# Kernel optimization log

Hardware: AMD Instinct MI355X
Metric: run time of the kernel (lower is better)

Reference implementation:

```python
import jax, jax.numpy as jnp
import numpy as np

D_MODEL = 256
SEQ_L = 4096
BATCH = 8
H = 3 * D_MODEL   # inner width after 3-branch concat
N_STATE = 32      # complex conjugate pairs -> d_state=64 real
KSIZES = (3, 7, 15)
DILATIONS = (1, 2, 4)


def setup_inputs() -> dict:
    k = jax.random.split(jax.random.key(0), 16)
    d = D_MODEL
    def w(ki, shape, scale):
        return jax.random.normal(ki, shape, jnp.float32) * scale
    inp = {"x": jax.random.normal(k[0], (BATCH, SEQ_L, d), jnp.float32)}
    for i, ksz in enumerate(KSIZES):
        inp[f"conv_w{i}"] = w(k[1 + i], (d, d, ksz), (d * ksz) ** -0.5)
        inp[f"conv_b{i}"] = jnp.zeros((d,), jnp.float32)
    inp["gate_w"] = w(k[4], (H, d), d ** -0.5)
    inp["gate_b"] = jnp.zeros((H,), jnp.float32)
    inp["res_w"] = w(k[5], (H, d), d ** -0.5)
    inp["res_b"] = jnp.zeros((H,), jnp.float32)
    # S4D (diagonal SSM) parameters, d_state=64 -> 32 complex pairs
    inp["log_dt"] = jax.random.uniform(k[6], (H,), jnp.float32, np.log(0.001), np.log(0.1))
    inp["A_re"] = -0.5 * jnp.ones((H, N_STATE), jnp.float32)
    inp["A_im"] = jnp.broadcast_to(np.pi * jnp.arange(N_STATE, dtype=jnp.float32), (H, N_STATE)).copy()
    inp["C_re"] = w(k[7], (H, N_STATE), 0.2)
    inp["C_im"] = w(k[8], (H, N_STATE), 0.2)
    inp["Dskip"] = jax.random.normal(k[9], (H,), jnp.float32)
    inp["ln_gamma"] = jnp.ones((H,), jnp.float32)
    inp["ln_beta"] = jnp.zeros((H,), jnp.float32)
    return inp


def _dil_conv(u, w, b, dil):
    # u: [B, C, L], w: [O, I, K], torch 'same' padding (odd kernels)
    y = jax.lax.conv_general_dilated(
        u, w, window_strides=(1,), padding="SAME", rhs_dilation=(dil,),
        dimension_numbers=("NCH", "OIH", "NCH"))
    return y + b[None, :, None]


def _s4d_apply(u, log_dt, A_re, A_im, C_re, C_im, Dskip):
    # u: [B, H, L]; diagonal SSM long convolution via FFT (ZOH discretization)
    L = u.shape[-1]
    dt = jnp.exp(log_dt)                          # [H]
    A = A_re + 1j * A_im                          # [H, N]
    C = C_re + 1j * C_im                          # [H, N]
    dtA = dt[:, None] * A                         # [H, N]
    C_disc = C * (jnp.exp(dtA) - 1.0) / A         # ZOH input matrix folded into C
    t = jnp.arange(L, dtype=jnp.float32)
    vand = jnp.exp(dtA[:, :, None] * t)           # [H, N, L] Vandermonde
    kern = 2.0 * jnp.real(jnp.einsum("hn,hnl->hl", C_disc, vand))  # [H, L]
    n_fft = 2 * L
    kf = jnp.fft.rfft(kern, n_fft)                # [H, n_fft/2+1]
    uf = jnp.fft.rfft(u, n_fft)                   # [B, H, n_fft/2+1]
    y = jnp.fft.irfft(uf * kf[None], n_fft)[..., :L]
    return y + Dskip[None, :, None] * u


def reference(x, conv_w0, conv_b0, conv_w1, conv_b1, conv_w2, conv_b2,
              gate_w, gate_b, res_w, res_b,
              log_dt, A_re, A_im, C_re, C_im, Dskip, ln_gamma, ln_beta):
    u = jnp.transpose(x, (0, 2, 1))               # [B, d, L]
    convs = [
        _dil_conv(u, conv_w0, conv_b0, DILATIONS[0]),
        _dil_conv(u, conv_w1, conv_b1, DILATIONS[1]),
        _dil_conv(u, conv_w2, conv_b2, DILATIONS[2]),
    ]
    combined = jnp.concatenate(convs, axis=1)     # [B, 3d, L]
    gate = jax.nn.sigmoid(jnp.einsum("bdl,od->bol", u, gate_w) + gate_b[None, :, None])
    gated = combined * gate
    s4_out = _s4d_apply(gated, log_dt, A_re, A_im, C_re, C_im, Dskip)
    resid = jnp.einsum("bdl,od->bol", u, res_w) + res_b[None, :, None]
    out = jnp.transpose(s4_out + resid, (0, 2, 1))  # [B, L, 3d]
    mu = jnp.mean(out, axis=-1, keepdims=True)
    var = jnp.mean((out - mu) ** 2, axis=-1, keepdims=True)
    return (out - mu) * jax.lax.rsqrt(var + 1e-5) * ln_gamma + ln_beta
```

## Files before the change

### kernel.cpp

```cpp
#include <hip/hip_runtime.h>
#include <cstdint>
#include <cstddef>


#define B_ 8
#define L_ 4096
#define D_ 256
#define H_ 768
#define NST 32
#define LC 128
#define NC 32

typedef _Float16 f16;
typedef _Float16 f16x8 __attribute__((ext_vector_type(8)));
typedef _Float16 f16x4 __attribute__((ext_vector_type(4)));
typedef _Float16 f16x2 __attribute__((ext_vector_type(2)));
typedef float f32x4 __attribute__((ext_vector_type(4)));

__device__ __forceinline__ f32x4 mfma16(f16x8 a, f16x8 b, f32x4 c) {
  return __builtin_amdgcn_mfma_f32_16x16x32_f16(a, b, c, 0, 0, 0);
}

#define GLDS16(g, l)                                                              \
  __builtin_amdgcn_global_load_lds((const __attribute__((address_space(1))) void*)(g), \
                                   (__attribute__((address_space(3))) void*)(l), 16, 0, 0)

__global__ __launch_bounds__(256) void prep_all(
    const float* __restrict__ x, const float* __restrict__ gate_w,
    const float* __restrict__ res_w,
    const float* __restrict__ w0, const float* __restrict__ w1, const float* __restrict__ w2,
    f16* __restrict__ xh, f16* __restrict__ Ag, float* __restrict__ zbuf,
    f16* __restrict__ A) {
  int bid = blockIdx.x, tid = threadIdx.x;
  if (bid < 8192) {
    int i = (bid * 256 + tid) * 4;
    float4 v = *(const float4*)(x + i);
    xh[i+0]=(f16)v.x; xh[i+1]=(f16)v.y; xh[i+2]=(f16)v.z; xh[i+3]=(f16)v.w;
  } else if (bid < 8384) {
    int i = ((bid - 8192) * 256 + tid) * 4;
    float4 v = *(const float4*)(gate_w + i);
    Ag[i+0]=(f16)v.x; Ag[i+1]=(f16)v.y; Ag[i+2]=(f16)v.z; Ag[i+3]=(f16)v.w;
  } else if (bid < 8576) {
    int i = ((bid - 8384) * 256 + tid) * 4;
    float4 v = *(const float4*)(res_w + i);
    f16* d = Ag + 768 * 256;
    d[i+0]=(f16)v.x; d[i+1]=(f16)v.y; d[i+2]=(f16)v.z; d[i+3]=(f16)v.w;
  } else if (bid == 8576) {
    zbuf[tid] = 0.f;
  } else {
    int idx = (bid - 8577) * 256 + tid;
    const int n0 = 256 * 256 * 3, n1 = 256 * 256 * 7;
    const float* w; int K, base;
    if (idx < n0) { w = w0; K = 3; base = 0; }
    else if (idx < n0 + n1) { idx -= n0; w = w1; K = 7; base = 256 * 768; }
    else { idx -= n0 + n1; w = w2; K = 15; base = 256 * 768 + 256 * 1792; }
    int o = idx / (256 * K); int r = idx - o * (256 * K); int j = r / K; int t = r - j * K;
    A[base + o * (256 * K) + t * 256 + j] = (f16)w[idx];
  }
}

__global__ __launch_bounds__(256) void s4_all(const float* __restrict__ log_dt,
                                              const float* __restrict__ A_re,
                                              const float* __restrict__ A_im,
                                              const float* __restrict__ C_re,
                                              const float* __restrict__ C_im,
                                              f16* __restrict__ A1, f16* __restrict__ A2,
                                              float* __restrict__ WLc,
                                              float* __restrict__ kT) {
  int bid = blockIdx.x, tid = threadIdx.x;
  if (bid < 96) {
    int idx = bid * 256 + tid;
    int h = idx >> 5, n = idx & 31;
    float dt = expf(log_dt[h]);
    float Ar = A_re[idx], Ai = A_im[idx];
    float ar = dt * Ar, ai = dt * Ai;
    float e = expf(ar), sn, cs; sincosf(ai, &sn, &cs);
    float wr = e * cs, wi = e * sn;
    float den = Ar * Ar + Ai * Ai;
    float Er = wr - 1.f, Ei = wi;
    float Cr = C_re[idx], Ci = C_im[idx];
    float nr = Cr * Er - Ci * Ei, ni = Cr * Ei + Ci * Er;
    float Cdr = (nr * Ar + ni * Ai) / den;
    float Cdi = (ni * Ar - nr * Ai) / den;
    f16* A1r = A1 + ((size_t)h * 64 + 2 * n) * LC;
    f16* A1i = A1 + ((size_t)h * 64 + 2 * n + 1) * LC;
    float pr = 1.f, pi = 0.f;
    for (int j = 0; j < LC; ++j) {
      A1r[LC - 1 - j] = (f16)pr; A1i[LC - 1 - j] = (f16)pi;
      float t0 = pr * wr - pi * wi; pi = pr * wi + pi * wr; pr = t0;
    }
    WLc[idx * 2] = pr; WLc[idx * 2 + 1] = pi;
    float qr = wr, qi = wi;
    for (int t = 0; t < LC; ++t) {
      A2[((size_t)h * LC + t) * 64 + 2 * n]     = (f16)(2.f * (Cdr * qr - Cdi * qi));
      A2[((size_t)h * LC + t) * 64 + 2 * n + 1] = (f16)(-2.f * (Cdr * qi + Cdi * qr));
      float t0 = qr * wr - qi * wi; qi = qr * wi + qi * wr; qr = t0;
    }
  } else {
    int idx = (bid - 96) * 256 + tid;
    int h = idx >> 7, j = idx & 127;
    float dt = expf(log_dt[h]);
    float acc = 0.f;
    for (int n = 0; n < NST; ++n) {
      float Ar = A_re[h * 32 + n], Ai = A_im[h * 32 + n];
      float ar = dt * Ar, ai = dt * Ai;
      float e1 = expf(ar), s1, c1; sincosf(ai, &s1, &c1);
      float wr = e1 * c1, wi = e1 * s1;
      float den = Ar * Ar + Ai * Ai;
      float Er = wr - 1.f, Ei = wi;
      float Cr = C_re[h * 32 + n], Ci = C_im[h * 32 + n];
      float nr = Cr * Er - Ci * Ei, ni = Cr * Ei + Ci * Er;
      float Cdr = (nr * Ar + ni * Ai) / den, Cdi = (ni * Ar - nr * Ai) / den;
      float ej = expf(ar * (float)j), sj, cj; sincosf(ai * (float)j, &sj, &cj);
      acc += 2.f * (Cdr * (ej * cj) - Cdi * (ej * sj));
    }
    kT[idx] = acc;
  }
}

__global__ __launch_bounds__(256) void gemm_gr(
    const f16* __restrict__ xh, const f16* __restrict__ Agr,
    const float* __restrict__ gate_b, const float* __restrict__ res_b,
    f16* __restrict__ gts, f16* __restrict__ res) {
  __shared__ f16 As[128 * 64];
  __shared__ f16 Bs[128 * 64];
  const int mt = blockIdx.y, nt = blockIdx.x;
  const int b = nt >> 5, l0 = (nt & 31) * 128;
  const bool isg = mt < 6;
  const int hbase = (isg ? mt : mt - 6) * 128;
  const f16* Abase = Agr + (size_t)((isg ? 0 : 768) + hbase) * 256;
  const int tid = threadIdx.x;
  const int wid = tid >> 6, lane = tid & 63, l15 = lane & 15, quad = lane >> 4;
  const int wm = (wid & 1) * 64, wn = (wid >> 1) * 64;
  const int srow = (wid << 5) + (lane >> 3);
  const int sperm = ((lane & 7) ^ (lane >> 3)) << 3;
  char* AsL = (char*)As + (wid << 12);
  char* BsL = (char*)Bs + (wid << 12);
  const f16* xrow = xh + (((size_t)b * L_) << 8);

  f32x4 acc[4][4];
#pragma unroll
  for (int i = 0; i < 4; ++i)
#pragma unroll
    for (int j = 0; j < 4; ++j) acc[i][j] = (f32x4){0.f, 0.f, 0.f, 0.f};

  for (int kc = 0; kc < 4; ++kc) {
#pragma unroll
    for (int j = 0; j < 4; ++j) {
      int row = srow + j * 8;
      GLDS16(Abase + (size_t)row * 256 + kc * 64 + sperm, AsL + (j << 10));
      GLDS16(xrow + ((size_t)(l0 + row) << 8) + kc * 64 + sperm, BsL + (j << 10));
    }
    __syncthreads();
#pragma unroll
    for (int k2 = 0; k2 < 2; ++k2) {
      f16x8 af[4], bf[4];
#pragma unroll
      for (int mi = 0; mi < 4; ++mi) {
        int r = wm + mi * 16 + l15;
        af[mi] = *(const f16x8*)(&As[r * 64 + (((k2 * 4 + quad) ^ (r & 7)) << 3)]);
      }
#pragma unroll
      for (int ni = 0; ni < 4; ++ni) {
        int r = wn + ni * 16 + l15;
        bf[ni] = *(const f16x8*)(&Bs[r * 64 + (((k2 * 4 + quad) ^ (r & 7)) << 3)]);
      }
#pragma unroll
      for (int mi = 0; mi < 4; ++mi)
#pragma unroll
        for (int ni = 0; ni < 4; ++ni) acc[mi][ni] = mfma16(af[mi], bf[ni], acc[mi][ni]);
    }
    __syncthreads();
  }

  if (isg) {
#pragma unroll
    for (int mi = 0; mi < 4; ++mi)
#pragma unroll
      for (int ni = 0; ni < 4; ++ni) {
        int hg = hbase + wm + mi * 16 + quad * 4;
        int lg = l0 + wn + ni * 16 + l15;
#pragma unroll
        for (int r = 0; r < 4; ++r) {
          float val = acc[mi][ni][r] + gate_b[hg + r];
          gts[((size_t)(b * H_ + hg + r)) * L_ + lg] = (f16)(1.f / (1.f + expf(-val)));
        }
      }
  } else {
#pragma unroll
    for (int mi = 0; mi < 4; ++mi)
#pragma unroll
      for (int ni = 0; ni < 4; ++ni) {
        int hg = hbase + wm + mi * 16 + quad * 4;
        int lg = l0 + wn + ni * 16 + l15;
#pragma unroll
        for (int r = 0; r < 4; ++r)
          res[((size_t)(b * H_ + hg + r)) * L_ + lg] = (f16)(acc[mi][ni][r] + res_b[hg + r]);
      }
  }
}

__global__ __launch_bounds__(512, 2) void gemm_conv8(
    const f16* __restrict__ xh, const f16* __restrict__ Aconv,
    const float* __restrict__ cb0, const float* __restrict__ cb1, const float* __restrict__ cb2,
    const f16* __restrict__ gts, const f16* __restrict__ zbuf,
    f16* __restrict__ v) {
  __shared__ f16 lds[69632];
  f16* Bs = lds + 49152;

  const int nt = blockIdx.x;
  const int b = nt >> 4, l0 = (nt & 15) * 256;
  const int ci = 2 - blockIdx.y;
  const int tid = threadIdx.x;
  const int wid = tid >> 6, lane = tid & 63, l15 = lane & 15, quad = lane >> 4;
  const int wr = wid >> 2, wc = wid & 3;
  const int rq = tid >> 3;
  const int cswz = ((tid & 7) ^ ((tid >> 3) & 7)) << 3;
  const f16* xrow = xh + (((size_t)b * L_) << 8);

  const f16* Acb; int Krow, taps, dil;
  if (ci == 0)      { Acb = Aconv;                          Krow = 768;  taps = 3;  dil = 1; }
  else if (ci == 1) { Acb = Aconv + 256 * 768;              Krow = 1792; taps = 7;  dil = 2; }
  else              { Acb = Aconv + 256 * 768 + 256 * 1792; Krow = 3840; taps = 15; dil = 4; }
  const int S = taps * 4;
  const int half = (taps - 1) / 2;

  f32x4 acc[8][4];
#pragma unroll
  for (int i = 0; i < 8; ++i)
#pragma unroll
    for (int j = 0; j < 4; ++j) acc[i][j] = (f32x4){0.f, 0.f, 0.f, 0.f};
  f16x8 af[4][2], blo[2][2], bhi[2][2];

  auto stageB = [&](int jc) {
#pragma unroll
    for (int q = 0; q < 5; ++q) {
      int r = q * 64 + rq;
      int gl = l0 - 32 + r;
      const f16* src = (gl < 0 || gl >= L_) ? (zbuf + cswz)
                       : xrow + ((size_t)gl << 8) + jc * 64 + cswz;
      GLDS16(src, Bs + q * 4096 + wid * 512);
    }
  };
  auto stageA2 = [&](int t2, int jc2, f16* buf, int q0) {
#pragma unroll
    for (int q = q0; q < q0 + 2; ++q) {
      const f16* src = Acb + (size_t)(q * 64 + rq) * Krow + t2 * 256 + jc2 * 64 + cswz;
      GLDS16(src, buf + q * 4096 + wid * 512);
    }
  };
  auto loadA = [&](const f16* Ab, int MH) {
#pragma unroll
    for (int mi = 0; mi < 4; ++mi) {
      int r = MH * 128 + wr * 64 + mi * 16 + l15;
#pragma unroll
      for (int k2 = 0; k2 < 2; ++k2)
        af[mi][k2] = *(const f16x8*)(Ab + r * 64 + (((k2 * 4 + quad) ^ (r & 7)) << 3));
    }
  };
  auto loadB = [&](int NH, int shift, f16x8 (&bf)[2][2]) {
#pragma unroll
    for (int ni = 0; ni < 2; ++ni) {
      int r = shift + NH * 128 + wc * 32 + ni * 16 + l15;
#pragma unroll
      for (int k2 = 0; k2 < 2; ++k2)
        bf[ni][k2] = *(const f16x8*)(Bs + r * 64 + (((k2 * 4 + quad) ^ (r & 7)) << 3));
    }
  };
  auto quadMM = [&](int MH, int NH, f16x8 (&bf)[2][2]) {
#pragma unroll
    for (int k2 = 0; k2 < 2; ++k2)
#pragma unroll
      for (int mi = 0; mi < 4; ++mi)
#pragma unroll
        for (int ni = 0; ni < 2; ++ni)
          acc[MH * 4 + mi][NH * 2 + ni] =
              mfma16(af[mi][k2], bf[ni][k2], acc[MH * 4 + mi][NH * 2 + ni]);
  };

  stageB(0);
  stageA2(0, 0, lds, 0);           stageA2(0, 0, lds, 2);
  stageA2(1, 0, lds + 16384, 0);   stageA2(1, 0, lds + 16384, 2);
  asm volatile("s_waitcnt vmcnt(0)" ::: "memory");
  __builtin_amdgcn_s_barrier();

  int s = 0, ca = 0;
#pragma unroll 1
  for (int jc = 0; jc < 4; ++jc) {
    if (jc > 0) {
      stageB(jc);
      asm volatile("s_waitcnt vmcnt(0)" ::: "memory");
      __builtin_amdgcn_s_barrier();
    }
#pragma unroll 1
    for (int t = 0; t < taps; ++t, ++s) {
      const int shift = 32 + (t - half) * dil;
      f16* Acur = lds + ca * 16384;
      int pa = ca - 1; if (pa < 0) pa = 2;
      f16* Apre = lds + pa * 16384;
      int t2 = t + 2, jc2 = jc;
      if (t2 >= taps) { t2 -= taps; ++jc2; }
      const bool pf = (jc2 < 4);
      loadA(Acur, 0); loadB(0, shift, blo);
      if (pf) stageA2(t2, jc2, Apre, 0);
      __builtin_amdgcn_s_barrier();
      asm volatile("s_waitcnt lgkmcnt(0)" ::: "memory");
      __builtin_amdgcn_s_setprio(1);
      quadMM(0, 0, blo);
      __builtin_amdgcn_s_setprio(0);
      __builtin_amdgcn_s_barrier();
      loadB(1, shift, bhi);
      if (pf) stageA2(t2, jc2, Apre, 2);
      __builtin_amdgcn_s_barrier();
      asm volatile("s_waitcnt lgkmcnt(0)" ::: "memory");
      __builtin_amdgcn_s_setprio(1);
      quadMM(0, 1, bhi);
      __builtin_amdgcn_s_setprio(0);
      __builtin_amdgcn_s_barrier();
      loadA(Acur, 1);
      __builtin_amdgcn_s_barrier();
      asm volatile("s_waitcnt lgkmcnt(0)" ::: "memory");
      __builtin_amdgcn_s_setprio(1);
      quadMM(1, 1, bhi);
      __builtin_amdgcn_s_setprio(0);
      __builtin_amdgcn_s_barrier();
      __builtin_amdgcn_s_setprio(1);
      quadMM(1, 0, blo);
      __builtin_amdgcn_s_setprio(0);
      if (pf) asm volatile("s_waitcnt vmcnt(4)" ::: "memory");
      else    asm volatile("s_waitcnt vmcnt(0)" ::: "memory");
      __builtin_amdgcn_s_barrier();
      ca = (ca == 2) ? 0 : ca + 1;
    }
  }

  const float* cbias = (ci == 0) ? cb0 : (ci == 1 ? cb1 : cb2);
#pragma unroll
  for (int mh = 0; mh < 2; ++mh)
#pragma unroll
    for (int mi = 0; mi < 4; ++mi)
#pragma unroll
      for (int nh = 0; nh < 2; ++nh)
#pragma unroll
        for (int ni = 0; ni < 2; ++ni) {
          int mg = mh * 128 + wr * 64 + mi * 16 + quad * 4;
          int lg = l0 + nh * 128 + wc * 32 + ni * 16 + l15;
          f32x4 a4 = acc[mh * 4 + mi][nh * 2 + ni];
#pragma unroll
          for (int r = 0; r < 4; ++r) {
            size_t a = ((size_t)(b * H_ + ci * 256 + mg + r)) * L_ + lg;
            float val = (a4[r] + cbias[mg + r]) * (float)gts[a];
            v[a] = (f16)val;
          }
        }
}

__global__ __launch_bounds__(256) void s1_states(const f16* __restrict__ v,
                                                 const f16* __restrict__ A1,
                                                 const float* __restrict__ WLc,
                                                 f16* __restrict__ Xin) {
  __shared__ f16 A1s[64 * 136];
  __shared__ f16 Vs[128 * 136];
  const int h = blockIdx.y, cb = blockIdx.x;
  const int tid = threadIdx.x;
  {
    int row = tid >> 2, q = tid & 3;
    const f16x8* src = (const f16x8*)(A1 + ((size_t)h * 64 + row) * 128 + q * 32);
    f16x8* dst = (f16x8*)(&A1s[row * 136 + q * 32]);
    dst[0] = src[0]; dst[1] = src[1]; dst[2] = src[2]; dst[3] = src[3];
  }
  {
    int col = tid >> 1, half = tid & 1;
    int cg = cb * 128 + col, b = cg >> 5, c = cg & 31;
    const f16x8* src = (const f16x8*)(v + ((size_t)(b * H_ + h)) * L_ + c * 128 + half * 64);
    f16x8* dst = (f16x8*)(&Vs[col * 136 + half * 64]);
    dst[0] = src[0]; dst[1] = src[1]; dst[2] = src[2]; dst[3] = src[3];
    dst[4] = src[4]; dst[5] = src[5]; dst[6] = src[6]; dst[7] = src[7];
  }
  __syncthreads();
  const int wid = tid >> 6, lane = tid & 63, l15 = lane & 15, quad = lane >> 4;
  const int n0 = wid * 32;
  f32x4 acc[4][2];
#pragma unroll
  for (int i = 0; i < 4; ++i) { acc[i][0] = (f32x4){0,0,0,0}; acc[i][1] = (f32x4){0,0,0,0}; }
#pragma unroll
  for (int bk = 0; bk < 4; ++bk) {
    f16x8 af[4], bf[2];
#pragma unroll
    for (int mi = 0; mi < 4; ++mi)
      af[mi] = *(const f16x8*)(&A1s[(mi * 16 + l15) * 136 + bk * 32 + quad * 8]);
#pragma unroll
    for (int ni = 0; ni < 2; ++ni)
      bf[ni] = *(const f16x8*)(&Vs[(n0 + ni * 16 + l15) * 136 + bk * 32 + quad * 8]);
#pragma unroll
    for (int mi = 0; mi < 4; ++mi)
#pragma unroll
      for (int ni = 0; ni < 2; ++ni) acc[mi][ni] = mfma16(af[mi], bf[ni], acc[mi][ni]);
  }
  __syncthreads();
  float* Xls = (float*)Vs;
#pragma unroll
  for (int mi = 0; mi < 4; ++mi)
#pragma unroll
    for (int ni = 0; ni < 2; ++ni) {
      int col = n0 + ni * 16 + l15;
      *(f32x4*)(&Xls[col * 68 + mi * 16 + quad * 4]) = acc[mi][ni];
    }
  __syncthreads();
  if (tid < 128) {
    int b4 = tid >> 5, n = tid & 31;
    int b = cb * 4 + b4;
    float Wr = WLc[(h * NST + n) * 2], Wi = WLc[(h * NST + n) * 2 + 1];
    float xr = 0.f, xi = 0.f;
    f16* xout = Xin + (((size_t)(b * H_ + h)) * NC) * 64 + 2 * n;
    for (int c = 0; c < NC; ++c) {
      float er = Xls[(b4 * 32 + c) * 68 + 2 * n];
      float ei = Xls[(b4 * 32 + c) * 68 + 2 * n + 1];
      f16x2 o; o[0] = (f16)xr; o[1] = (f16)xi;
      *(f16x2*)(xout + (size_t)c * 64) = o;
      float t = Wr * xr - Wi * xi + er;
      xi = Wr * xi + Wi * xr + ei; xr = t;
    }
  }
}

__global__ __launch_bounds__(256) void s3_output(const f16* __restrict__ v,
                                                 const f16* __restrict__ A2g,
                                                 const f16* __restrict__ res,
                                                 const float* __restrict__ kT,
                                                 const f16* __restrict__ Xin,
                                                 const float* __restrict__ Dskip,
                                                 f16* __restrict__ y4) {
  __shared__ f16 Ts[128 * 136];
  __shared__ f16 Vs[64 * 136];
  __shared__ float kTs[128];
  f16* A2s = Ts;
  f16* Xs = Ts + 128 * 72;
  const int h = blockIdx.y, cb = blockIdx.x;
  const int tid = threadIdx.x;
  if (tid < 128) kTs[tid] = kT[h * 128 + tid];
  {
    int col = tid >> 2, q = tid & 3;
    int cg = cb * 64 + col, b = cg >> 5, c = cg & 31;
    const f16x8* src = (const f16x8*)(v + ((size_t)(b * H_ + h)) * L_ + c * 128 + q * 32);
    f16x8* dst = (f16x8*)(&Vs[col * 136 + q * 32]);
    dst[0] = src[0]; dst[1] = src[1]; dst[2] = src[2]; dst[3] = src[3];
  }
  __syncthreads();
  {
    int tau = tid >> 1, h64 = (tid & 1) * 64;
#pragma unroll
    for (int jv = 0; jv < 8; ++jv) {
      int s0 = h64 + jv * 8;
      f16x8 w;
#pragma unroll
      for (int e = 0; e < 8; ++e) {
        int s = s0 + e;
        w[e] = (f16)((s <= tau) ? kTs[tau - s] : 0.f);
      }
      *(f16x8*)(&Ts[tau * 136 + s0]) = w;
    }
  }
  __syncthreads();
  const int wid = tid >> 6, lane = tid & 63, l15 = lane & 15, quad = lane >> 4;
  const int wm = (wid & 1) * 64, wn = (wid >> 1) * 32;
  f32x4 acc[4][2];
#pragma unroll
  for (int i = 0; i < 4; ++i) { acc[i][0] = (f32x4){0,0,0,0}; acc[i][1] = (f32x4){0,0,0,0}; }
#pragma unroll
  for (int bk = 0; bk < 4; ++bk) {
    f16x8 af[4], bf[2];
#pragma unroll
    for (int mi = 0; mi < 4; ++mi)
      af[mi] = *(const f16x8*)(&Ts[(wm + mi * 16 + l15) * 136 + bk * 32 + quad * 8]);
#pragma unroll
    for (int ni = 0; ni < 2; ++ni)
      bf[ni] = *(const f16x8*)(&Vs[(wn + ni * 16 + l15) * 136 + bk * 32 + quad * 8]);
#pragma unroll
    for (int mi = 0; mi < 4; ++mi)
#pragma unroll
      for (int ni = 0; ni < 2; ++ni) acc[mi][ni] = mfma16(af[mi], bf[ni], acc[mi][ni]);
  }
  __syncthreads();
  {
    int row = tid >> 1, half = tid & 1;
    const f16x8* src = (const f16x8*)(A2g + ((size_t)h * 128 + row) * 64 + half * 32);
    f16x8* dst = (f16x8*)(&A2s[row * 72 + half * 32]);
    dst[0] = src[0]; dst[1] = src[1]; dst[2] = src[2]; dst[3] = src[3];
  }
  {
    int col = tid >> 2, part = tid & 3;
    int cg = cb * 64 + col, b = cg >> 5, c = cg & 31;
    const f16x8* src = (const f16x8*)(Xin + (((size_t)(b * H_ + h)) * NC + c) * 64 + part * 16);
    f16x8* dst = (f16x8*)(&Xs[col * 72 + part * 16]);
    dst[0] = src[0]; dst[1] = src[1];
  }
  __syncthreads();
#pragma unroll
  for (int bk = 0; bk < 2; ++bk) {
    f16x8 af[4], bf[2];
#pragma unroll
    for (int mi = 0; mi < 4; ++mi)
      af[mi] = *(const f16x8*)(&A2s[(wm + mi * 16 + l15) * 72 + bk * 32 + quad * 8]);
#pragma unroll
    for (int ni = 0; ni < 2; ++ni)
      bf[ni] = *(const f16x8*)(&Xs[(wn + ni * 16 + l15) * 72 + bk * 32 + quad * 8]);
#pragma unroll
    for (int mi = 0; mi < 4; ++mi)
#pragma unroll
      for (int ni = 0; ni < 2; ++ni) acc[mi][ni] = mfma16(af[mi], bf[ni], acc[mi][ni]);
  }
  float Dh = Dskip[h];
#pragma unroll
  for (int mi = 0; mi < 4; ++mi)
#pragma unroll
    for (int ni = 0; ni < 2; ++ni) {
      int col = wn + ni * 16 + l15;
      int cg = cb * 64 + col, b = cg >> 5, c = cg & 31;
      int tau0 = wm + mi * 16 + quad * 4;
      size_t lbase = ((size_t)(b * H_ + h)) * L_ + c * 128 + tau0;
      const f16* rp = res + lbase;
      f16x4 o;
#pragma unroll
      for (int r = 0; r < 4; ++r)
        o[r] = (f16)(acc[mi][ni][r] + Dh * (float)Vs[col * 136 + tau0 + r] + (float)rp[r]);
      *(f16x4*)(y4 + lbase) = o;
    }
}

__global__ __launch_bounds__(256) void layernorm_t(const f16* __restrict__ y4,
                                                   const float* __restrict__ gamma,
                                                   const float* __restrict__ beta,
                                                   float* __restrict__ out) {
  __shared__ f16 Ys[768 * 72];
  __shared__ float psum[256], psq[256], mu[64], rs[64];
  const int b = blockIdx.y, l0 = blockIdx.x * 64;
  const int tid = threadIdx.x;
  {
    int r8 = tid >> 3, c = tid & 7;
    for (int it = 0; it < 24; ++it) {
      int hh = it * 32 + r8;
      f16x8 x = *(const f16x8*)(y4 + ((size_t)(b * H_ + hh)) * L_ + l0 + c * 8);
      *(f16x8*)(&Ys[hh * 72 + c * 8]) = x;
    }
  }
  __syncthreads();
  {
    int l = tid & 63, hg = tid >> 6;
    float s = 0.f, s2 = 0.f;
    for (int k = 0; k < 192; ++k) {
      float val = (float)Ys[(hg * 192 + k) * 72 + l];
      s += val; s2 += val * val;
    }
    psum[hg * 64 + l] = s; psq[hg * 64 + l] = s2;
  }
  __syncthreads();
  if (tid < 64) {
    float S = 0.f, S2 = 0.f;
    for (int g = 0; g < 4; ++g) { S += psum[g * 64 + tid]; S2 += psq[g * 64 + tid]; }
    float m = S / 768.f;
    float var = S2 / 768.f - m * m;
    mu[tid] = m; rs[tid] = rsqrtf(var + 1e-5f);
  }
  __syncthreads();
  float g0 = gamma[tid], g1 = gamma[256 + tid], g2 = gamma[512 + tid];
  float be0 = beta[tid], be1 = beta[256 + tid], be2 = beta[512 + tid];
  for (int lv = 0; lv < 8; ++lv) {
    f16x8 y0 = *(const f16x8*)(&Ys[(size_t)tid * 72 + lv * 8]);
    f16x8 y1 = *(const f16x8*)(&Ys[(size_t)(256 + tid) * 72 + lv * 8]);
    f16x8 y2 = *(const f16x8*)(&Ys[(size_t)(512 + tid) * 72 + lv * 8]);
#pragma unroll
    for (int e = 0; e < 8; ++e) {
      int ll = lv * 8 + e;
      float m = mu[ll], r = rs[ll];
      size_t ob = ((size_t)b * L_ + l0 + ll) * H_;
      out[ob + tid]       = ((float)y0[e] - m) * r * g0 + be0;
      out[ob + 256 + tid] = ((float)y1[e] - m) * r * g1 + be1;
      out[ob + 512 + tid] = ((float)y2[e] - m) * r * g2 + be2;
    }
  }
}

extern "C" void kernel_launch(void* const* d_in, const int* in_sizes, int n_in,
                              void* d_out, int out_size, void* d_ws, size_t ws_size,
                              hipStream_t stream) {
  const float* x      = (const float*)d_in[0];
  const float* cw0    = (const float*)d_in[1];
  const float* cb0    = (const float*)d_in[2];
  const float* cw1    = (const float*)d_in[3];
  const float* cb1    = (const float*)d_in[4];
  const float* cw2    = (const float*)d_in[5];
  const float* cb2    = (const float*)d_in[6];
  const float* gate_w = (const float*)d_in[7];
  const float* gate_b = (const float*)d_in[8];
  const float* res_w  = (const float*)d_in[9];
  const float* res_b  = (const float*)d_in[10];
  const float* log_dt = (const float*)d_in[11];
  const float* A_re   = (const float*)d_in[12];
  const float* A_im   = (const float*)d_in[13];
  const float* C_re   = (const float*)d_in[14];
  const float* C_im   = (const float*)d_in[15];
  const float* Dskip  = (const float*)d_in[16];
  const float* ln_g   = (const float*)d_in[17];
  const float* ln_b   = (const float*)d_in[18];
  float* out = (float*)d_out;

  char* ws = (char*)d_ws;
  f16*   xh   = (f16*)(ws + 0);
  f16*   Ac   = (f16*)(ws + 16777216);
  f16*   Ag   = (f16*)(ws + 20054016);
  f16*   zbuf = (f16*)(ws + 20840448);
  f16*   vb   = (f16*)(ws + 20841472);
  f16*   resb = (f16*)(ws + 71173120);
  f16*   gts  = (f16*)(ws + 121504768);
  f16*   A1   = (f16*)(ws + 171836416);
  f16*   A2   = (f16*)(ws + 184419328);
  float* kT   = (float*)(ws + 197002240);
  float* WLc  = (float*)(ws + 197395456);
  f16*   Xin  = (f16*)(ws + 197592064);
  f16*   y4   = (f16*)(ws + 222757888);

  prep_all<<<14977, 256, 0, stream>>>(x, gate_w, res_w, cw0, cw1, cw2,
                                      xh, Ag, (float*)zbuf, Ac);
  s4_all<<<480, 256, 0, stream>>>(log_dt, A_re, A_im, C_re, C_im, A1, A2, WLc, kT);

  gemm_gr<<<dim3(256, 12), 256, 0, stream>>>(xh, Ag, gate_b, res_b, gts, resb);
  gemm_conv8<<<dim3(128, 3), 512, 0, stream>>>(xh, Ac, cb0, cb1, cb2, gts, zbuf, vb);

  s1_states<<<dim3(2, 768), 256, 0, stream>>>(vb, A1, WLc, Xin);
  s3_output<<<dim3(4, 768), 256, 0, stream>>>(vb, A2, resb, kT, Xin, Dskip, y4);

  layernorm_t<<<dim3(64, 8), 256, 0, stream>>>(y4, ln_g, ln_b, out);
}
```

Before: 453.6 us.

## Remap conv GEMM warps to 4x2 tiling and software-pipeline B fragment reads

```diff
diff --git a/kernel.cpp b/kernel.cpp
--- a/kernel.cpp
+++ b/kernel.cpp
@@ -213,7 +213,7 @@
   const int ci = 2 - blockIdx.y;
   const int tid = threadIdx.x;
   const int wid = tid >> 6, lane = tid & 63, l15 = lane & 15, quad = lane >> 4;
-  const int wr = wid >> 2, wc = wid & 3;
+  const int wr = wid >> 1, wc = wid & 1;
   const int rq = tid >> 3;
   const int cswz = ((tid & 7) ^ ((tid >> 3) & 7)) << 3;
   const f16* xrow = xh + (((size_t)b * L_) << 8);
@@ -222,15 +222,15 @@
   if (ci == 0)      { Acb = Aconv;                          Krow = 768;  taps = 3;  dil = 1; }
   else if (ci == 1) { Acb = Aconv + 256 * 768;              Krow = 1792; taps = 7;  dil = 2; }
   else              { Acb = Aconv + 256 * 768 + 256 * 1792; Krow = 3840; taps = 15; dil = 4; }
-  const int S = taps * 4;
   const int half = (taps - 1) / 2;
-
-  f32x4 acc[8][4];
-#pragma unroll
-  for (int i = 0; i < 8; ++i)
-#pragma unroll
-    for (int j = 0; j < 4; ++j) acc[i][j] = (f32x4){0.f, 0.f, 0.f, 0.f};
-  f16x8 af[4][2], blo[2][2], bhi[2][2];
+  const int shift0 = 32 - half * dil;
+
+  f32x4 acc[4][8];
+#pragma unroll
+  for (int i = 0; i < 4; ++i)
+#pragma unroll
+    for (int j = 0; j < 8; ++j) acc[i][j] = (f32x4){0.f, 0.f, 0.f, 0.f};
+  f16x8 af[4][2], bfA[2][2], bfB[2][2];
 
   auto stageB = [&](int jc) {
 #pragma unroll
@@ -242,117 +242,104 @@
       GLDS16(src, Bs + q * 4096 + wid * 512);
     }
   };
-  auto stageA2 = [&](int t2, int jc2, f16* buf, int q0) {
-#pragma unroll
-    for (int q = q0; q < q0 + 2; ++q) {
+  auto stageA4 = [&](int t2, int jc2, f16* buf) {
+#pragma unroll
+    for (int q = 0; q < 4; ++q) {
       const f16* src = Acb + (size_t)(q * 64 + rq) * Krow + t2 * 256 + jc2 * 64 + cswz;
       GLDS16(src, buf + q * 4096 + wid * 512);
     }
   };
-  auto loadA = [&](const f16* Ab, int MH) {
+  auto readAF = [&](const f16* Ab) {
 #pragma unroll
     for (int mi = 0; mi < 4; ++mi) {
-      int r = MH * 128 + wr * 64 + mi * 16 + l15;
+      int r = wr * 64 + mi * 16 + l15;
 #pragma unroll
       for (int k2 = 0; k2 < 2; ++k2)
         af[mi][k2] = *(const f16x8*)(Ab + r * 64 + (((k2 * 4 + quad) ^ (r & 7)) << 3));
     }
   };
-  auto loadB = [&](int NH, int shift, f16x8 (&bf)[2][2]) {
+  auto readBF = [&](int q, int shift, f16x8 (&bf)[2][2]) {
 #pragma unroll
     for (int ni = 0; ni < 2; ++ni) {
-      int r = shift + NH * 128 + wc * 32 + ni * 16 + l15;
+      int r = shift + wc * 128 + q * 32 + ni * 16 + l15;
 #pragma unroll
       for (int k2 = 0; k2 < 2; ++k2)
         bf[ni][k2] = *(const f16x8*)(Bs + r * 64 + (((k2 * 4 + quad) ^ (r & 7)) << 3));
     }
   };
-  auto quadMM = [&](int MH, int NH, f16x8 (&bf)[2][2]) {
+  auto qMM = [&](int q, f16x8 (&bf)[2][2]) {
 #pragma unroll
     for (int k2 = 0; k2 < 2; ++k2)
 #pragma unroll
       for (int mi = 0; mi < 4; ++mi)
 #pragma unroll
         for (int ni = 0; ni < 2; ++ni)
-          acc[MH * 4 + mi][NH * 2 + ni] =
-              mfma16(af[mi][k2], bf[ni][k2], acc[MH * 4 + mi][NH * 2 + ni]);
+          acc[mi][q * 2 + ni] = mfma16(af[mi][k2], bf[ni][k2], acc[mi][q * 2 + ni]);
   };
 
   stageB(0);
-  stageA2(0, 0, lds, 0);           stageA2(0, 0, lds, 2);
-  stageA2(1, 0, lds + 16384, 0);   stageA2(1, 0, lds + 16384, 2);
+  stageA4(0, 0, lds);
+  stageA4(1, 0, lds + 16384);
   asm volatile("s_waitcnt vmcnt(0)" ::: "memory");
   __builtin_amdgcn_s_barrier();
-
-  int s = 0, ca = 0;
+  readBF(0, shift0, bfA);
+
+  int ca = 0;
 #pragma unroll 1
   for (int jc = 0; jc < 4; ++jc) {
-    if (jc > 0) {
-      stageB(jc);
-      asm volatile("s_waitcnt vmcnt(0)" ::: "memory");
-      __builtin_amdgcn_s_barrier();
-    }
 #pragma unroll 1
-    for (int t = 0; t < taps; ++t, ++s) {
-      const int shift = 32 + (t - half) * dil;
+    for (int t = 0; t < taps; ++t) {
+      const int shift = shift0 + t * dil;
       f16* Acur = lds + ca * 16384;
-      int pa = ca - 1; if (pa < 0) pa = 2;
+      int pa = ca + 2; if (pa >= 3) pa -= 3;
       f16* Apre = lds + pa * 16384;
       int t2 = t + 2, jc2 = jc;
       if (t2 >= taps) { t2 -= taps; ++jc2; }
       const bool pf = (jc2 < 4);
-      loadA(Acur, 0); loadB(0, shift, blo);
-      if (pf) stageA2(t2, jc2, Apre, 0);
-      __builtin_amdgcn_s_barrier();
-      asm volatile("s_waitcnt lgkmcnt(0)" ::: "memory");
-      __builtin_amdgcn_s_setprio(1);
-      quadMM(0, 0, blo);
-      __builtin_amdgcn_s_setprio(0);
-      __builtin_amdgcn_s_barrier();
-      loadB(1, shift, bhi);
-      if (pf) stageA2(t2, jc2, Apre, 2);
-      __builtin_amdgcn_s_barrier();
-      asm volatile("s_waitcnt lgkmcnt(0)" ::: "memory");
-      __builtin_amdgcn_s_setprio(1);
-      quadMM(0, 1, bhi);
-      __builtin_amdgcn_s_setprio(0);
-      __builtin_amdgcn_s_barrier();
-      loadA(Acur, 1);
-      __builtin_amdgcn_s_barrier();
-      asm volatile("s_waitcnt lgkmcnt(0)" ::: "memory");
-      __builtin_amdgcn_s_setprio(1);
-      quadMM(1, 1, bhi);
-      __builtin_amdgcn_s_setprio(0);
-      __builtin_amdgcn_s_barrier();
-      __builtin_amdgcn_s_setprio(1);
-      quadMM(1, 0, blo);
-      __builtin_amdgcn_s_setprio(0);
-      if (pf) asm volatile("s_waitcnt vmcnt(4)" ::: "memory");
-      else    asm volatile("s_waitcnt vmcnt(0)" ::: "memory");
-      __builtin_amdgcn_s_barrier();
+
+      readAF(Acur);
+      readBF(1, shift, bfB);
+      if (pf) stageA4(t2, jc2, Apre);
+      qMM(0, bfA);
+      readBF(2, shift, bfA);
+      qMM(1, bfB);
+      readBF(3, shift, bfB);
+      qMM(2, bfA);
+      qMM(3, bfB);
+
+      if (t < taps - 1) {
+        readBF(0, shift + dil, bfA);
+        if (pf) asm volatile("s_waitcnt vmcnt(4)" ::: "memory");
+        else    asm volatile("s_waitcnt vmcnt(0)" ::: "memory");
+        __builtin_amdgcn_s_barrier();
+      } else if (jc < 3) {
+        __builtin_amdgcn_s_barrier();
+        stageB(jc + 1);
+        asm volatile("s_waitcnt vmcnt(0)" ::: "memory");
+        __builtin_amdgcn_s_barrier();
+        readBF(0, shift0, bfA);
+      }
       ca = (ca == 2) ? 0 : ca + 1;
     }
   }
 
   const float* cbias = (ci == 0) ? cb0 : (ci == 1 ? cb1 : cb2);
 #pragma unroll
-  for (int mh = 0; mh < 2; ++mh)
-#pragma unroll
-    for (int mi = 0; mi < 4; ++mi)
-#pragma unroll
-      for (int nh = 0; nh < 2; ++nh)
-#pragma unroll
-        for (int ni = 0; ni < 2; ++ni) {
-          int mg = mh * 128 + wr * 64 + mi * 16 + quad * 4;
-          int lg = l0 + nh * 128 + wc * 32 + ni * 16 + l15;
-          f32x4 a4 = acc[mh * 4 + mi][nh * 2 + ni];
-#pragma unroll
-          for (int r = 0; r < 4; ++r) {
-            size_t a = ((size_t)(b * H_ + ci * 256 + mg + r)) * L_ + lg;
-            float val = (a4[r] + cbias[mg + r]) * (float)gts[a];
-            v[a] = (f16)val;
-          }
+  for (int mi = 0; mi < 4; ++mi)
+#pragma unroll
+    for (int q = 0; q < 4; ++q)
+#pragma unroll
+      for (int ni = 0; ni < 2; ++ni) {
+        int mg = wr * 64 + mi * 16 + quad * 4;
+        int lg = l0 + wc * 128 + q * 32 + ni * 16 + l15;
+        f32x4 a4 = acc[mi][q * 2 + ni];
+#pragma unroll
+        for (int r = 0; r < 4; ++r) {
+          size_t a = ((size_t)(b * H_ + ci * 256 + mg + r)) * L_ + lg;
+          float val = (a4[r] + cbias[mg + r]) * (float)gts[a];
+          v[a] = (f16)val;
         }
+      }
 }
 
 __global__ __launch_bounds__(256) void s1_states(const f16* __restrict__ v,
```

New measurement: 441.8 us. 1.03x faster.
